# Optimization experiments

Hardware: AMD Instinct MI355X
Metric: run time of the kernel (lower is better)

## Reference

```python
import jax, jax.numpy as jnp
import numpy as np

SEQ_DIM = 256
PAIR_DIM = 128
HIDDEN = 32
B, L = 1, 384
EPS = 1e-5


def setup_inputs() -> dict:
    key = jax.random.key(0)
    ks = jax.random.split(key, 8)
    # xavier-normal-ish scales for the linear weights
    def xn(k, shape):
        fan_in, fan_out = shape[1], shape[0]
        std = (2.0 / (fan_in + fan_out)) ** 0.5
        return jax.random.normal(k, shape, dtype=jnp.float32) * std
    return {
        "seq": jax.random.normal(ks[0], (B, L, SEQ_DIM), dtype=jnp.float32),
        "ln_gamma": jnp.ones((SEQ_DIM,), dtype=jnp.float32),
        "ln_beta": jnp.zeros((SEQ_DIM,), dtype=jnp.float32),
        "w1": xn(ks[1], (HIDDEN, SEQ_DIM)),
        "b1": jnp.zeros((HIDDEN,), dtype=jnp.float32),
        "w2": xn(ks[2], (HIDDEN, SEQ_DIM)),
        "b2": jnp.zeros((HIDDEN,), dtype=jnp.float32),
        "w3": xn(ks[3], (PAIR_DIM, HIDDEN * HIDDEN)),
        "b3": jnp.zeros((PAIR_DIM,), dtype=jnp.float32),
    }


def reference(seq, ln_gamma, ln_beta, w1, b1, w2, b2, w3, b3):
    # LayerNorm over last dim (eps matches torch default 1e-5)
    mu = jnp.mean(seq, axis=-1, keepdims=True)
    var = jnp.mean(jnp.square(seq - mu), axis=-1, keepdims=True)
    x = (seq - mu) * jax.lax.rsqrt(var + EPS) * ln_gamma + ln_beta

    s1 = x @ w1.T + b1  # [B, L, H]
    s2 = x @ w2.T + b2  # [B, L, H]

    # pair[b,i,j,p] = sum_{d,f} s1[b,i,d] * s2[b,j,f] * w3[p, d*H+f] + b3[p]
    # Equivalent to einsum('bid,bjf->bijdf') -> view -> Linear, but contracted
    # directly without materializing the [B,L,L,H*H] intermediate.
    w3r = w3.reshape(PAIR_DIM, HIDDEN, HIDDEN)
    pair = jnp.einsum('bid,bjf,pdf->bijp', s1, s2, w3r) + b3
    return pair
```

## Files before the change

kernel.cpp:

```cpp
#include <hip/hip_runtime.h>
#include <hip/hip_bf16.h>


typedef __attribute__((ext_vector_type(8))) short short8;
typedef __attribute__((ext_vector_type(4))) float f32x4;

static __device__ __forceinline__ short f2bf(float f) {
    unsigned u = __float_as_uint(f);
    unsigned r = u + 0x7fffu + ((u >> 16) & 1u);
    return (short)(r >> 16);
}

static __device__ __forceinline__ void store_out(float* D, size_t idx, float v) { D[idx] = v; }
static __device__ __forceinline__ void store_out(short* D, size_t idx, float v) { D[idx] = f2bf(v); }

__global__ __launch_bounds__(256) void cast_bf16_kernel(const float* __restrict__ in,
                                                        short* __restrict__ out, int n) {
    int i = blockIdx.x * 256 + threadIdx.x;
    if (i < n) out[i] = f2bf(in[i]);
}

__global__ __launch_bounds__(256) void ln_proj_kernel(
    const float* __restrict__ seq, const float* __restrict__ gamma,
    const float* __restrict__ beta, const float* __restrict__ w1,
    const float* __restrict__ b1, const float* __restrict__ w2,
    const float* __restrict__ b2, short* __restrict__ s1, short* __restrict__ s2) {
    const int row = blockIdx.x;
    const int t = threadIdx.x;
    const int wv = t >> 6;
    const int ln = t & 63;

    __shared__ float wsum[4];
    __shared__ float xln[256];
    __shared__ float part[4][64];

    float v = seq[row * 256 + t];

    float s = v;
    #pragma unroll
    for (int off = 32; off > 0; off >>= 1) s += __shfl_down(s, off);
    if (ln == 0) wsum[wv] = s;
    __syncthreads();
    float mean = (wsum[0] + wsum[1] + wsum[2] + wsum[3]) * (1.0f / 256.0f);

    float c = v - mean;
    float cs = c * c;
    #pragma unroll
    for (int off = 32; off > 0; off >>= 1) cs += __shfl_down(cs, off);
    __syncthreads();
    if (ln == 0) wsum[wv] = cs;
    __syncthreads();
    float var = (wsum[0] + wsum[1] + wsum[2] + wsum[3]) * (1.0f / 256.0f);

    float xn = c * rsqrtf(var + 1e-5f) * gamma[t] + beta[t];
    xln[t] = xn;
    __syncthreads();

    const float* w = (ln < 32) ? (w1 + ln * 256) : (w2 + (ln - 32) * 256);
    const float* xs = &xln[wv * 64];
    const float* wp = w + wv * 64;
    float p = 0.0f;
    #pragma unroll 8
    for (int i = 0; i < 64; ++i) p += xs[i] * wp[i];
    part[wv][ln] = p;
    __syncthreads();

    if (t < 64) {
        float r = part[0][t] + part[1][t] + part[2][t] + part[3][t];
        if (t < 32) { r += b1[t];      s1[row * 32 + t]        = f2bf(r); }
        else        { r += b2[t - 32]; s2[row * 32 + (t - 32)] = f2bf(r); }
    }
}

template <typename OutT, bool BIAS>
__global__ __launch_bounds__(256, 4) void gemm_k32_kernel(
    const short* __restrict__ A, const short* __restrict__ B,
    OutT* __restrict__ D, const float* __restrict__ bias, int M, int N) {
    const int lane = threadIdx.x & 63;
    const int wave = threadIdx.x >> 6;
    const int l15  = lane & 15;
    const int quad = lane >> 4;
    const int k0   = quad * 8;
    const int n    = blockIdx.x * 64 + wave * 16 + l15;

    short8 bfrag = *reinterpret_cast<const short8*>(B + (size_t)n * 32 + k0);
    float bv = 0.0f;
    if (BIAS) bv = bias[n & 127];

    const int mchunk = M / gridDim.y;
    const int mbeg = blockIdx.y * mchunk;
    const int mend = mbeg + mchunk;

    const short* aptr = A + (size_t)(mbeg + l15) * 32 + k0;
    size_t dbase = (size_t)(mbeg + quad * 4) * N + n;
    const size_t dstep = (size_t)16 * N;

    for (int m0 = mbeg; m0 < mend; m0 += 16) {
        short8 afrag = *reinterpret_cast<const short8*>(aptr);
        f32x4 acc = {0.0f, 0.0f, 0.0f, 0.0f};
        acc = __builtin_amdgcn_mfma_f32_16x16x32_bf16(afrag, bfrag, acc, 0, 0, 0);
        #pragma unroll
        for (int r = 0; r < 4; ++r)
            store_out(D, dbase + (size_t)r * N, acc[r] + bv);
        aptr += 16 * 32;
        dbase += dstep;
    }
}

extern "C" void kernel_launch(void* const* d_in, const int* in_sizes, int n_in,
                              void* d_out, int out_size, void* d_ws, size_t ws_size,
                              hipStream_t stream) {
    const float* seq   = (const float*)d_in[0];
    const float* gamma = (const float*)d_in[1];
    const float* beta  = (const float*)d_in[2];
    const float* w1    = (const float*)d_in[3];
    const float* b1    = (const float*)d_in[4];
    const float* w2    = (const float*)d_in[5];
    const float* b2    = (const float*)d_in[6];
    const float* w3    = (const float*)d_in[7];
    const float* b3    = (const float*)d_in[8];
    float* out = (float*)d_out;

    const int L = 384, H = 32, P = 128;
    const int N2 = P * H;
    const int N3 = L * P;

    char* ws = (char*)d_ws;
    short* s1  = (short*)(ws);
    short* s2  = (short*)(ws + 24576);
    short* w3c = (short*)(ws + 49152);
    short* T   = (short*)(ws + 311296);

    cast_bf16_kernel<<<(P * H * H + 255) / 256, 256, 0, stream>>>(w3, w3c, P * H * H);

    ln_proj_kernel<<<L, 256, 0, stream>>>(seq, gamma, beta, w1, b1, w2, b2, s1, s2);

    gemm_k32_kernel<short, false><<<dim3(N2 / 64, 4), 256, 0, stream>>>(
        s2, w3c, T, nullptr, L, N2);

    gemm_k32_kernel<float, true><<<dim3(N3 / 64, 2), 256, 0, stream>>>(
        s1, T, out, b3, L, N3);
}
```

Baseline: 114.4 us.

## Swap MFMA operands for vectorized stores, fuse weight cast into LN kernel

The GEMM now swaps the MFMA A/B operands so each lane holds four consecutive output columns. Each lane can then write one 16-byte nontemporal float4 store (or one 8-byte bf16x4 store) instead of four strided scalar stores. The A fragment is prefetched one iteration ahead, and the M-loop trip counts become compile-time constants (3 and 12), with the first GEMM's grid split further. The separate w3 cast kernel is folded into the LayerNorm/projection launch as extra blocks, and the projection loop reads weights as float4. The main target is store efficiency on the large fp32 output write, at the cost of hard-coding shapes.

```diff
diff --git a/kernel.cpp b/kernel.cpp
--- a/kernel.cpp
+++ b/kernel.cpp
@@ -3,6 +3,7 @@
 
 
 typedef __attribute__((ext_vector_type(8))) short short8;
+typedef __attribute__((ext_vector_type(4))) short bf16x4;
 typedef __attribute__((ext_vector_type(4))) float f32x4;
 
 static __device__ __forceinline__ short f2bf(float f) {
@@ -11,22 +12,22 @@
     return (short)(r >> 16);
 }
 
-static __device__ __forceinline__ void store_out(float* D, size_t idx, float v) { D[idx] = v; }
-static __device__ __forceinline__ void store_out(short* D, size_t idx, float v) { D[idx] = f2bf(v); }
-
-__global__ __launch_bounds__(256) void cast_bf16_kernel(const float* __restrict__ in,
-                                                        short* __restrict__ out, int n) {
-    int i = blockIdx.x * 256 + threadIdx.x;
-    if (i < n) out[i] = f2bf(in[i]);
-}
-
-__global__ __launch_bounds__(256) void ln_proj_kernel(
+__global__ __launch_bounds__(256) void ln_proj_cast_kernel(
     const float* __restrict__ seq, const float* __restrict__ gamma,
     const float* __restrict__ beta, const float* __restrict__ w1,
     const float* __restrict__ b1, const float* __restrict__ w2,
-    const float* __restrict__ b2, short* __restrict__ s1, short* __restrict__ s2) {
+    const float* __restrict__ b2, const float* __restrict__ w3,
+    short* __restrict__ s1, short* __restrict__ s2, short* __restrict__ w3c,
+    int L) {
+    const int t = threadIdx.x;
+
+    if (blockIdx.x >= L) {
+        int i = (blockIdx.x - L) * 256 + t;
+        w3c[i] = f2bf(w3[i]);
+        return;
+    }
+
     const int row = blockIdx.x;
-    const int t = threadIdx.x;
     const int wv = t >> 6;
     const int ln = t & 63;
 
@@ -57,11 +58,15 @@
     __syncthreads();
 
     const float* w = (ln < 32) ? (w1 + ln * 256) : (w2 + (ln - 32) * 256);
+    const f32x4* wp = (const f32x4*)(w + wv * 64);
     const float* xs = &xln[wv * 64];
-    const float* wp = w + wv * 64;
     float p = 0.0f;
-    #pragma unroll 8
-    for (int i = 0; i < 64; ++i) p += xs[i] * wp[i];
+    #pragma unroll
+    for (int i = 0; i < 16; ++i) {
+        f32x4 w4 = wp[i];
+        p += xs[4*i + 0] * w4.x + xs[4*i + 1] * w4.y +
+             xs[4*i + 2] * w4.z + xs[4*i + 3] * w4.w;
+    }
     part[wv][ln] = p;
     __syncthreads();
 
@@ -72,38 +77,46 @@
     }
 }
 
-template <typename OutT, bool BIAS>
+template <typename OutT, bool BIAS, int MITERS>
 __global__ __launch_bounds__(256, 4) void gemm_k32_kernel(
     const short* __restrict__ A, const short* __restrict__ B,
-    OutT* __restrict__ D, const float* __restrict__ bias, int M, int N) {
+    OutT* __restrict__ D, const float* __restrict__ bias, int N) {
     const int lane = threadIdx.x & 63;
     const int wave = threadIdx.x >> 6;
     const int l15  = lane & 15;
     const int quad = lane >> 4;
     const int k0   = quad * 8;
-    const int n    = blockIdx.x * 64 + wave * 16 + l15;
+    const int n0   = blockIdx.x * 64 + wave * 16;
+    const int mbeg = blockIdx.y * (MITERS * 16);
 
-    short8 bfrag = *reinterpret_cast<const short8*>(B + (size_t)n * 32 + k0);
-    float bv = 0.0f;
-    if (BIAS) bv = bias[n & 127];
+    short8 bfrag = *reinterpret_cast<const short8*>(B + (size_t)(n0 + l15) * 32 + k0);
 
-    const int mchunk = M / gridDim.y;
-    const int mbeg = blockIdx.y * mchunk;
-    const int mend = mbeg + mchunk;
+    f32x4 bv = {0.0f, 0.0f, 0.0f, 0.0f};
+    if (BIAS) bv = *reinterpret_cast<const f32x4*>(bias + ((n0 + quad * 4) & 127));
 
     const short* aptr = A + (size_t)(mbeg + l15) * 32 + k0;
-    size_t dbase = (size_t)(mbeg + quad * 4) * N + n;
+    OutT* dptr = D + (size_t)(mbeg + l15) * N + n0 + quad * 4;
     const size_t dstep = (size_t)16 * N;
 
-    for (int m0 = mbeg; m0 < mend; m0 += 16) {
-        short8 afrag = *reinterpret_cast<const short8*>(aptr);
+    short8 a_cur = *reinterpret_cast<const short8*>(aptr);
+    #pragma unroll
+    for (int it = 0; it < MITERS; ++it) {
+        aptr += 16 * 32;
+        short8 a_nxt;
+        if (it + 1 < MITERS) a_nxt = *reinterpret_cast<const short8*>(aptr);
+
         f32x4 acc = {0.0f, 0.0f, 0.0f, 0.0f};
-        acc = __builtin_amdgcn_mfma_f32_16x16x32_bf16(afrag, bfrag, acc, 0, 0, 0);
-        #pragma unroll
-        for (int r = 0; r < 4; ++r)
-            store_out(D, dbase + (size_t)r * N, acc[r] + bv);
-        aptr += 16 * 32;
-        dbase += dstep;
+        acc = __builtin_amdgcn_mfma_f32_16x16x32_bf16(bfrag, a_cur, acc, 0, 0, 0);
+
+        if constexpr (BIAS) acc += bv;
+        if constexpr (sizeof(OutT) == 4) {
+            __builtin_nontemporal_store(acc, (f32x4*)dptr);
+        } else {
+            bf16x4 pv = { f2bf(acc.x), f2bf(acc.y), f2bf(acc.z), f2bf(acc.w) };
+            *reinterpret_cast<bf16x4*>(dptr) = pv;
+        }
+        dptr += dstep;
+        a_cur = a_nxt;
     }
 }
 
@@ -131,13 +144,12 @@
     short* w3c = (short*)(ws + 49152);
     short* T   = (short*)(ws + 311296);
 
-    cast_bf16_kernel<<<(P * H * H + 255) / 256, 256, 0, stream>>>(w3, w3c, P * H * H);
+    ln_proj_cast_kernel<<<L + (P * H * H) / 256, 256, 0, stream>>>(
+        seq, gamma, beta, w1, b1, w2, b2, w3, s1, s2, w3c, L);
 
-    ln_proj_kernel<<<L, 256, 0, stream>>>(seq, gamma, beta, w1, b1, w2, b2, s1, s2);
+    gemm_k32_kernel<short, false, 3><<<dim3(N2 / 64, 8), 256, 0, stream>>>(
+        s2, w3c, T, nullptr, N2);
 
-    gemm_k32_kernel<short, false><<<dim3(N2 / 64, 4), 256, 0, stream>>>(
-        s2, w3c, T, nullptr, L, N2);
-
-    gemm_k32_kernel<float, true><<<dim3(N3 / 64, 2), 256, 0, stream>>>(
-        s1, T, out, b3, L, N3);
+    gemm_k32_kernel<float, true, 12><<<dim3(N3 / 64, 2), 256, 0, stream>>>(
+        s1, T, out, b3, N3);
 }
```

After: 118.1 us. 3.2% more time.
